# Kernel tuning notes

Measured on AMD Instinct MI355X. Metric: run time of the kernel, lower is better.

The kernel has to match this reference:

```python
import jax, jax.numpy as jnp
import numpy as np

B, N, DIN, DINNER, DOUT, W = 4, 8192, 512, 512, 512, 128


def setup_inputs() -> dict:
    key = jax.random.key(0)
    k1, k2, k3 = jax.random.split(key, 3)
    x = jax.random.normal(k1, (B, N, DIN), jnp.float32)
    # torch Linear weights: (out_features, in_features)
    w_qkv = jax.random.normal(k2, (3 * DINNER, DIN), jnp.float32) * (DIN ** -0.5)
    w_out = jax.random.normal(k3, (DOUT, DINNER), jnp.float32) * (DINNER ** -0.5)
    b_out = jnp.zeros((DOUT,), jnp.float32)
    return {"x": x, "w_qkv": w_qkv, "w_out": w_out, "b_out": b_out}


def reference(x, w_qkv, w_out, b_out):
    b, n, _ = x.shape
    w = W
    scale = DINNER ** -0.5
    pad = (-n) % w  # pad_to_multiple along seq dim (static)
    xp = jnp.pad(x, ((0, 0), (0, pad), (0, 0)))
    qkv = jnp.einsum('bnd,ed->bne', xp, w_qkv)  # to_qkv, no bias
    q, k, v = jnp.split(qkv, 3, axis=-1)
    win = lambda t: t.reshape(b, -1, w, DINNER)  # b (w n) d -> b w n d
    q, k, v = win(q), win(k), win(v)
    # prepend one zero bucket to k, then overlap prev/current windows.
    kp = jnp.pad(k, ((0, 0), (1, 0), (0, 0), (0, 0)))
    k2 = jnp.concatenate((kp[:, :-1], kp[:, 1:]), axis=2)  # (b, nb, 2w, d)
    # NOTE: source bug replicated — v is also built from k, not v.
    v2 = jnp.concatenate((kp[:, :-1], kp[:, 1:]), axis=2)
    sim = jnp.einsum('bwid,bwjd->bwij', q, k2) * scale  # (b, nb, w, 2w)
    i, j = w, 2 * w
    mask = jnp.triu(jnp.ones((i, j), bool), j - i + 1)
    sim = jnp.where(mask, -jnp.finfo(sim.dtype).max, sim)
    attn = jax.nn.softmax(sim, axis=-1)
    out = jnp.einsum('bwij,bwjd->bwid', attn, v2)
    out = out.reshape(b, -1, DINNER)[:, :n]
    return jnp.einsum('bnd,od->bno', out, w_out) + b_out
```

## Files before the change

kernel.cpp:

```cpp
#include <hip/hip_runtime.h>
#include <cstdint>
#include <cstddef>

typedef float f32x4 __attribute__((ext_vector_type(4)));
typedef short s16x8 __attribute__((ext_vector_type(8)));
typedef short s16x4 __attribute__((ext_vector_type(4)));

#define MFMA_BF16(a, b, c) __builtin_amdgcn_mfma_f32_16x16x32_bf16((a), (b), (c), 0, 0, 0)

#define GLD16(g, l)                                                            \
  __builtin_amdgcn_global_load_lds(                                            \
      (const __attribute__((address_space(1))) void*)(g),                      \
      (__attribute__((address_space(3))) void*)(l), 16, 0, 0)

__device__ __forceinline__ unsigned short f2bf(float f) {
  unsigned int u = __float_as_uint(f);
  u += 0x7FFFu + ((u >> 16) & 1u);
  return (unsigned short)(u >> 16);
}

__device__ __forceinline__ s16x8 cvt8(const float* __restrict__ src) {
  const float4 f0 = *(const float4*)src;
  const float4 f1 = *(const float4*)(src + 4);
  s16x8 h;
  h[0] = (short)f2bf(f0.x); h[1] = (short)f2bf(f0.y);
  h[2] = (short)f2bf(f0.z); h[3] = (short)f2bf(f0.w);
  h[4] = (short)f2bf(f1.x); h[5] = (short)f2bf(f1.y);
  h[6] = (short)f2bf(f1.z); h[7] = (short)f2bf(f1.w);
  return h;
}

#define XN 16777216
#define WQN 524288
__global__ __launch_bounds__(256)
void cvt_bf16(const float* __restrict__ x, const float* __restrict__ wqkv,
              const float* __restrict__ wout, unsigned short* __restrict__ xb,
              unsigned short* __restrict__ wb, unsigned short* __restrict__ wob) {
  const size_t i = (size_t)(blockIdx.x * 256 + threadIdx.x) * 8;
  const float* src;
  unsigned short* dst;
  if (i < XN) { src = x + i; dst = xb + i; }
  else if (i < XN + WQN) { src = wqkv + (i - XN); dst = wb + (i - XN); }
  else { src = wout + (i - XN - WQN); dst = wob + (i - XN - WQN); }
  *(s16x8*)dst = cvt8(src);
}

__global__ __launch_bounds__(256)
void gemm_qk(const unsigned short* __restrict__ xb, const unsigned short* __restrict__ wb,
             unsigned short* __restrict__ Q, unsigned short* __restrict__ K) {
  __shared__ unsigned short As[128 * 64];
  __shared__ unsigned short Bs[128 * 64];
  const int t = threadIdx.x, lane = t & 63, wid = t >> 6;
  const int wm = wid >> 1, wn = wid & 1;
  const int nl = lane & 15, quad = lane >> 4;
  const int sub = lane >> 3, lblk = (lane & 7) ^ sub;
  const int l = blockIdx.x;
  const int xcd = l & 7, g = l >> 3;
  const int mt = (g >> 3) * 8 + xcd, nt = g & 7;
  const int m0 = mt * 128, n0 = nt * 128;

  const f32x4 zero = {0.f, 0.f, 0.f, 0.f};
  f32x4 acc[4][4];
#pragma unroll
  for (int i = 0; i < 4; ++i)
#pragma unroll
    for (int j = 0; j < 4; ++j) acc[i][j] = zero;

  const unsigned short* gX = xb + (size_t)(m0 + wid * 32 + sub) * 512 + lblk * 8;
  const unsigned short* gW = wb + (size_t)(n0 + wid * 32 + sub) * 512 + lblk * 8;

  for (int kc = 0; kc < 512; kc += 64) {
#pragma unroll
    for (int ii = 0; ii < 4; ++ii) {
      GLD16(gW + kc + (size_t)(ii * 8) * 512, &As[(wid * 32 + ii * 8) * 64]);
      GLD16(gX + kc + (size_t)(ii * 8) * 512, &Bs[(wid * 32 + ii * 8) * 64]);
    }
    __syncthreads();
#pragma unroll
    for (int ks = 0; ks < 2; ++ks) {
      s16x8 af[4], bf[4];
#pragma unroll
      for (int i = 0; i < 4; ++i)
        af[i] = *(const s16x8*)&As[(wm * 64 + i * 16 + nl) * 64 +
                                   (((ks * 4 + quad) ^ (nl & 7)) * 8)];
#pragma unroll
      for (int j = 0; j < 4; ++j)
        bf[j] = *(const s16x8*)&Bs[(wn * 64 + j * 16 + nl) * 64 +
                                   (((ks * 4 + quad) ^ (nl & 7)) * 8)];
#pragma unroll
      for (int i = 0; i < 4; ++i)
#pragma unroll
        for (int j = 0; j < 4; ++j) acc[i][j] = MFMA_BF16(af[i], bf[j], acc[i][j]);
    }
    __syncthreads();
  }
#pragma unroll
  for (int i = 0; i < 4; ++i) {
    const int n = n0 + wm * 64 + i * 16 + quad * 4;
    unsigned short* base = (n < 512 ? Q : K);
    const int nn = n & 511;
#pragma unroll
    for (int j = 0; j < 4; ++j) {
      const int m = m0 + wn * 64 + j * 16 + nl;
      s16x4 h;
#pragma unroll
      for (int r = 0; r < 4; ++r) h[r] = (short)f2bf(acc[i][j][r]);
      *(s16x4*)&base[(size_t)m * 512 + nn] = h;
    }
  }
}

__global__ __launch_bounds__(256)
void gemm_kwt(const unsigned short* __restrict__ K, const unsigned short* __restrict__ wob,
              unsigned short* __restrict__ KWT) {
  __shared__ unsigned short As[128 * 64];
  __shared__ unsigned short Bs[128 * 64];
  const int t = threadIdx.x, lane = t & 63, wid = t >> 6;
  const int wm = wid >> 1, wn = wid & 1;
  const int nl = lane & 15, quad = lane >> 4;
  const int sub = lane >> 3, lblk = (lane & 7) ^ sub;
  const int l = blockIdx.x;
  const int xcd = l & 7, g = l >> 3;
  const int mt = (g >> 2) * 8 + xcd, nt = g & 3;
  const int m0 = mt * 128, n0 = nt * 128;

  const f32x4 zero = {0.f, 0.f, 0.f, 0.f};
  f32x4 acc[4][4];
#pragma unroll
  for (int i = 0; i < 4; ++i)
#pragma unroll
    for (int j = 0; j < 4; ++j) acc[i][j] = zero;

  const unsigned short* gA = K + (size_t)(m0 + wid * 32 + sub) * 512 + lblk * 8;
  const unsigned short* gB = wob + (size_t)(n0 + wid * 32 + sub) * 512 + lblk * 8;

  for (int kc = 0; kc < 512; kc += 64) {
#pragma unroll
    for (int ii = 0; ii < 4; ++ii) {
      GLD16(gA + kc + (size_t)(ii * 8) * 512, &As[(wid * 32 + ii * 8) * 64]);
      GLD16(gB + kc + (size_t)(ii * 8) * 512, &Bs[(wid * 32 + ii * 8) * 64]);
    }
    __syncthreads();
#pragma unroll
    for (int ks = 0; ks < 2; ++ks) {
      s16x8 af[4], bf[4];
#pragma unroll
      for (int i = 0; i < 4; ++i)
        af[i] = *(const s16x8*)&As[(wm * 64 + i * 16 + nl) * 64 +
                                   (((ks * 4 + quad) ^ (nl & 7)) * 8)];
#pragma unroll
      for (int j = 0; j < 4; ++j)
        bf[j] = *(const s16x8*)&Bs[(wn * 64 + j * 16 + nl) * 64 +
                                   (((ks * 4 + quad) ^ (nl & 7)) * 8)];
#pragma unroll
      for (int i = 0; i < 4; ++i)
#pragma unroll
        for (int j = 0; j < 4; ++j) acc[i][j] = MFMA_BF16(af[i], bf[j], acc[i][j]);
    }
    __syncthreads();
  }
#pragma unroll
  for (int i = 0; i < 4; ++i) {
    const int ms = m0 + wm * 64 + i * 16 + quad * 4;
    const int b = ms >> 13, ns = ms & 8191;
#pragma unroll
    for (int j = 0; j < 4; ++j) {
      const int o = n0 + wn * 64 + j * 16 + nl;
      s16x4 h;
#pragma unroll
      for (int r = 0; r < 4; ++r) h[r] = (short)f2bf(acc[i][j][r]);
      *(s16x4*)&KWT[(size_t)(b * 512 + o) * 8192 + ns] = h;
    }
  }
}

__global__ __launch_bounds__(256)
void attn64(const unsigned short* __restrict__ Q, const unsigned short* __restrict__ K,
            const unsigned short* __restrict__ KWT, const float* __restrict__ bias,
            float* __restrict__ out) {
  __shared__ __align__(16) char smem[73728];
  unsigned short* const Qb  = (unsigned short*)smem;
  unsigned short* const Kbo = (unsigned short*)(smem + 8192);
  unsigned short* const Kbe = (unsigned short*)(smem + 40960);
  unsigned short* const Ps  = (unsigned short*)smem;
  float* const redm = (float*)(smem + 32768);
  float* const reds = (float*)(smem + 33792);
  unsigned short* const B20 = (unsigned short*)(smem + 40960);
  unsigned short* const B21 = (unsigned short*)(smem + 57344);

  const int t = threadIdx.x, lane = t & 63, wid = t >> 6;
  const int wn = wid;
  const int nl = lane & 15, quad = lane >> 4;
  const int sub = lane >> 3, lblk = (lane & 7) ^ sub;
  const int bx = blockIdx.x;
  const int xcd = bx & 7, half = (bx >> 3) & 1, g = bx >> 4;
  const int wb = g * 8 + xcd, b = wb >> 6, w = wb & 63;

  const unsigned short* Qg = Q + (size_t)(b * 8192 + w * 128 + half * 64) * 512;
  const unsigned short* Kg = K + (size_t)(b * 8192) * 512;
  const unsigned short* KWTb = KWT + (size_t)(b * 512) * 8192;
  const int seqbase = w * 128 - 128;

#define STAGE_Q(kcc)                                                           \
  do {                                                                         \
    _Pragma("unroll") for (int ii = 0; ii < 2; ++ii)                           \
        GLD16(Qg + (size_t)(wid * 16 + ii * 8 + sub) * 512 + (kcc) + lblk * 8, \
              Qb + (wid * 16 + ii * 8) * 64);                                  \
  } while (0)

#define STAGE_K(kcc, kb)                                                       \
  do {                                                                         \
    _Pragma("unroll") for (int ii = 0; ii < 8; ++ii) {                         \
      int sq_ = seqbase + wid * 64 + ii * 8 + sub;                             \
      if (sq_ < 0) sq_ = 0;                                                    \
      GLD16(Kg + (size_t)sq_ * 512 + (kcc) + lblk * 8,                         \
            (kb) + (wid * 64 + ii * 8) * 64);                                  \
    }                                                                          \
  } while (0)

#define STAGE_B2(tt, bb)                                                       \
  do {                                                                         \
    const int och_ = (tt) >> 2, kch_ = (tt) & 3;                               \
    int sq_ = seqbase + kch_ * 64 + lblk * 8;                                  \
    if (sq_ < 0) sq_ = 0;                                                      \
    _Pragma("unroll") for (int ii = 0; ii < 4; ++ii)                           \
        GLD16(KWTb + (size_t)(och_ * 128 + wid * 32 + ii * 8 + sub) * 8192 + sq_, \
              (bb) + (wid * 32 + ii * 8) * 64);                                \
  } while (0)

  float bo[4][2];
#pragma unroll
  for (int och = 0; och < 4; ++och)
#pragma unroll
    for (int j = 0; j < 2; ++j) bo[och][j] = bias[och * 128 + wn * 32 + j * 16 + nl];

  const f32x4 zero = {0.f, 0.f, 0.f, 0.f};
  f32x4 acc[4][4];
#pragma unroll
  for (int i = 0; i < 4; ++i)
#pragma unroll
    for (int j = 0; j < 4; ++j) acc[i][j] = zero;

  STAGE_K(0, Kbe);
  STAGE_Q(0);
#pragma unroll
  for (int s = 0; s < 8; ++s) {
    unsigned short* const kb = (s & 1) ? Kbo : Kbe;
    if (s < 7) {
      STAGE_K((s + 1) * 64, (s & 1) ? Kbe : Kbo);
      asm volatile("s_waitcnt vmcnt(8)" ::: "memory");
    } else {
      STAGE_B2(0, B20);
      asm volatile("s_waitcnt vmcnt(4)" ::: "memory");
    }
    __builtin_amdgcn_s_barrier();
    asm volatile("" ::: "memory");
#pragma unroll
    for (int ks = 0; ks < 2; ++ks) {
      s16x8 af[4], bf[4];
#pragma unroll
      for (int i = 0; i < 4; ++i)
        af[i] = *(const s16x8*)&Qb[(i * 16 + nl) * 64 +
                                   (((ks * 4 + quad) ^ (nl & 7)) * 8)];
#pragma unroll
      for (int j = 0; j < 4; ++j)
        bf[j] = *(const s16x8*)&kb[(wn * 64 + j * 16 + nl) * 64 +
                                   (((ks * 4 + quad) ^ (nl & 7)) * 8)];
      __builtin_amdgcn_s_setprio(1);
#pragma unroll
      for (int i = 0; i < 4; ++i)
#pragma unroll
        for (int j = 0; j < 4; ++j) acc[i][j] = MFMA_BF16(af[i], bf[j], acc[i][j]);
      __builtin_amdgcn_s_setprio(0);
    }
    asm volatile("" ::: "memory");
    __builtin_amdgcn_s_barrier();
    if (s < 7) STAGE_Q((s + 1) * 64);
  }
  STAGE_B2(1, B21);

  const float scale = 0.04419417382415922f;
  float rmax[4][4];
#pragma unroll
  for (int i = 0; i < 4; ++i) {
#pragma unroll
    for (int r = 0; r < 4; ++r) {
      const int qrow = half * 64 + i * 16 + quad * 4 + r;
      float mx = -3.4e38f;
#pragma unroll
      for (int j = 0; j < 4; ++j) {
        const int col = wn * 64 + j * 16 + nl;
        float v = acc[i][j][r] * scale;
        if (col >= 128 && col - 128 > qrow) v = -3.0e38f;
        if (w == 0 && col < 128) v = 0.0f;
        acc[i][j][r] = v;
        mx = fmaxf(mx, v);
      }
      rmax[i][r] = mx;
    }
  }
#pragma unroll
  for (int off = 1; off < 16; off <<= 1)
#pragma unroll
    for (int i = 0; i < 4; ++i)
#pragma unroll
      for (int r = 0; r < 4; ++r)
        rmax[i][r] = fmaxf(rmax[i][r], __shfl_xor(rmax[i][r], off, 64));
  if (nl == 0) {
#pragma unroll
    for (int i = 0; i < 4; ++i)
#pragma unroll
      for (int r = 0; r < 4; ++r)
        redm[(i * 16 + quad * 4 + r) * 4 + wn] = rmax[i][r];
  }
  asm volatile("s_waitcnt lgkmcnt(0)" ::: "memory");
  __builtin_amdgcn_s_barrier();
  asm volatile("" ::: "memory");
  float rsum[4][4];
#pragma unroll
  for (int i = 0; i < 4; ++i) {
#pragma unroll
    for (int r = 0; r < 4; ++r) {
      const f32x4 mv = *(const f32x4*)&redm[(i * 16 + quad * 4 + r) * 4];
      const float m = fmaxf(fmaxf(mv[0], mv[1]), fmaxf(mv[2], mv[3]));
      float s = 0.f;
#pragma unroll
      for (int j = 0; j < 4; ++j) {
        const float p = __expf(acc[i][j][r] - m);
        acc[i][j][r] = p;
        s += p;
      }
      rsum[i][r] = s;
    }
  }
#pragma unroll
  for (int off = 1; off < 16; off <<= 1)
#pragma unroll
    for (int i = 0; i < 4; ++i)
#pragma unroll
      for (int r = 0; r < 4; ++r) rsum[i][r] += __shfl_xor(rsum[i][r], off, 64);
  if (nl == 0) {
#pragma unroll
    for (int i = 0; i < 4; ++i)
#pragma unroll
      for (int r = 0; r < 4; ++r)
        reds[(i * 16 + quad * 4 + r) * 4 + wn] = rsum[i][r];
  }
  asm volatile("s_waitcnt lgkmcnt(0)" ::: "memory");
  __builtin_amdgcn_s_barrier();
  asm volatile("" ::: "memory");
  float invv[4][4];
#pragma unroll
  for (int i = 0; i < 4; ++i)
#pragma unroll
    for (int r = 0; r < 4; ++r) {
      const f32x4 sv = *(const f32x4*)&reds[(i * 16 + quad * 4 + r) * 4];
      invv[i][r] = 1.0f / (sv[0] + sv[1] + sv[2] + sv[3]);
    }
  asm volatile("s_waitcnt lgkmcnt(0)" ::: "memory");
  __builtin_amdgcn_s_barrier();
  asm volatile("" ::: "memory");
#pragma unroll
  for (int i = 0; i < 4; ++i) {
#pragma unroll
    for (int r = 0; r < 4; ++r) {
      const int row = i * 16 + quad * 4 + r;
#pragma unroll
      for (int j = 0; j < 4; ++j) {
        const int col = wn * 64 + j * 16 + nl;
        float pv = acc[i][j][r] * invv[i][r];
        if (w == 0 && col < 128) pv = 0.0f;
        const int cb = col >> 3;
        Ps[row * 256 + (((cb ^ (row & 7)) << 3) | (col & 7))] = f2bf(pv);
      }
    }
  }
  asm volatile("s_waitcnt lgkmcnt(0)" ::: "memory");
  __builtin_amdgcn_s_barrier();
  asm volatile("" ::: "memory");

  f32x4 acc2[4][2];
#pragma unroll
  for (int t2 = 0; t2 < 16; ++t2) {
    const int och = t2 >> 2, kch = t2 & 3;
    unsigned short* const bb = (t2 & 1) ? B21 : B20;
    if (kch == 0) {
#pragma unroll
      for (int i = 0; i < 4; ++i)
#pragma unroll
        for (int j = 0; j < 2; ++j) acc2[i][j] = zero;
    }
    if (t2 < 15) asm volatile("s_waitcnt vmcnt(4)" ::: "memory");
    else         asm volatile("s_waitcnt vmcnt(0)" ::: "memory");
    __builtin_amdgcn_s_barrier();
    asm volatile("" ::: "memory");
#pragma unroll
    for (int ks = 0; ks < 2; ++ks) {
      const int kb2 = kch * 8 + ks * 4 + quad;
      s16x8 af[4], bf[2];
#pragma unroll
      for (int i = 0; i < 4; ++i)
        af[i] = *(const s16x8*)&Ps[(i * 16 + nl) * 256 + ((kb2 ^ (nl & 7)) << 3)];
#pragma unroll
      for (int j = 0; j < 2; ++j)
        bf[j] = *(const s16x8*)&bb[(wn * 32 + j * 16 + nl) * 64 +
                                   (((ks * 4 + quad) ^ (nl & 7)) * 8)];
      __builtin_amdgcn_s_setprio(1);
#pragma unroll
      for (int i = 0; i < 4; ++i) {
        acc2[i][0] = MFMA_BF16(af[i], bf[0], acc2[i][0]);
        acc2[i][1] = MFMA_BF16(af[i], bf[1], acc2[i][1]);
      }
      __builtin_amdgcn_s_setprio(0);
    }
    asm volatile("" ::: "memory");
    __builtin_amdgcn_s_barrier();
    if (kch == 3) {
#pragma unroll
      for (int i = 0; i < 4; ++i) {
        const int seq = w * 128 + half * 64 + i * 16 + quad * 4;
        float* dst = out + (size_t)(b * 8192 + seq) * 512;
#pragma unroll
        for (int j = 0; j < 2; ++j) {
          const int o = och * 128 + wn * 32 + j * 16 + nl;
#pragma unroll
          for (int r = 0; r < 4; ++r) dst[(size_t)r * 512 + o] = acc2[i][j][r] + bo[och][j];
        }
      }
    }
    if (t2 < 14) STAGE_B2(t2 + 2, bb);
  }
#undef STAGE_Q
#undef STAGE_K
#undef STAGE_B2
}

extern "C" void kernel_launch(void* const* d_in, const int* in_sizes, int n_in,
                              void* d_out, int out_size, void* d_ws, size_t ws_size,
                              hipStream_t stream) {
  const float* x = (const float*)d_in[0];
  const float* w_qkv = (const float*)d_in[1];
  const float* w_out = (const float*)d_in[2];
  const float* b_out = (const float*)d_in[3];
  float* out = (float*)d_out;

  char* ws = (char*)d_ws;
  unsigned short* Q = (unsigned short*)ws;
  unsigned short* K = (unsigned short*)(ws + (size_t)33554432);
  unsigned short* xb = (unsigned short*)(ws + (size_t)67108864);
  unsigned short* KWT = (unsigned short*)(ws + (size_t)67108864);
  unsigned short* wb = (unsigned short*)(ws + (size_t)100663296);
  unsigned short* wob = (unsigned short*)(ws + (size_t)100663296 + 1048576);

  cvt_bf16<<<dim3(8576), dim3(256), 0, stream>>>(x, w_qkv, w_out, xb, wb, wob);
  gemm_qk<<<dim3(2048), dim3(256), 0, stream>>>(xb, wb, Q, K);
  gemm_kwt<<<dim3(1024), dim3(256), 0, stream>>>(K, wob, KWT);
  attn64<<<dim3(512), dim3(256), 0, stream>>>(Q, K, KWT, b_out, out);
}
```

Baseline: 234.5 us.

## Fuse fp32-to-bf16 conversion of x into QK GEMM with register prefetch

The separate pass that converted x to bf16 is removed. The QK GEMM now loads fp32 x directly into registers, converts it, and writes it into LDS, prefetching the next K-chunk while the current one computes. The weight-only conversion stays as a small kernel. This saves a full write and re-read of a 32 MB bf16 copy of x, but each GEMM block now re-reads fp32 x once per N-tile (8 tiles), adds conversion ALU work and register pressure inside the GEMM, and uses manual waitcnt and barriers plus setprio around the MFMAs.

```diff
diff --git a/kernel.cpp b/kernel.cpp
--- a/kernel.cpp
+++ b/kernel.cpp
@@ -30,23 +30,29 @@
   return h;
 }
 
-#define XN 16777216
+__device__ __forceinline__ s16x8 cvt8r(float4 f0, float4 f1) {
+  s16x8 h;
+  h[0] = (short)f2bf(f0.x); h[1] = (short)f2bf(f0.y);
+  h[2] = (short)f2bf(f0.z); h[3] = (short)f2bf(f0.w);
+  h[4] = (short)f2bf(f1.x); h[5] = (short)f2bf(f1.y);
+  h[6] = (short)f2bf(f1.z); h[7] = (short)f2bf(f1.w);
+  return h;
+}
+
 #define WQN 524288
 __global__ __launch_bounds__(256)
-void cvt_bf16(const float* __restrict__ x, const float* __restrict__ wqkv,
-              const float* __restrict__ wout, unsigned short* __restrict__ xb,
-              unsigned short* __restrict__ wb, unsigned short* __restrict__ wob) {
+void cvt_w(const float* __restrict__ wqkv, const float* __restrict__ wout,
+           unsigned short* __restrict__ wb, unsigned short* __restrict__ wob) {
   const size_t i = (size_t)(blockIdx.x * 256 + threadIdx.x) * 8;
   const float* src;
   unsigned short* dst;
-  if (i < XN) { src = x + i; dst = xb + i; }
-  else if (i < XN + WQN) { src = wqkv + (i - XN); dst = wb + (i - XN); }
-  else { src = wout + (i - XN - WQN); dst = wob + (i - XN - WQN); }
+  if (i < WQN) { src = wqkv + i; dst = wb + i; }
+  else { src = wout + (i - WQN); dst = wob + (i - WQN); }
   *(s16x8*)dst = cvt8(src);
 }
 
 __global__ __launch_bounds__(256)
-void gemm_qk(const unsigned short* __restrict__ xb, const unsigned short* __restrict__ wb,
+void gemm_qk(const float* __restrict__ x, const unsigned short* __restrict__ wb,
              unsigned short* __restrict__ Q, unsigned short* __restrict__ K) {
   __shared__ unsigned short As[128 * 64];
   __shared__ unsigned short Bs[128 * 64];
@@ -66,16 +72,36 @@
 #pragma unroll
     for (int j = 0; j < 4; ++j) acc[i][j] = zero;
 
-  const unsigned short* gX = xb + (size_t)(m0 + wid * 32 + sub) * 512 + lblk * 8;
+  const float* gXf = x + (size_t)(m0 + wid * 32 + sub) * 512 + lblk * 8;
   const unsigned short* gW = wb + (size_t)(n0 + wid * 32 + sub) * 512 + lblk * 8;
 
+  float4 rx[4][2];
+#define LOADX(kcc)                                                             \
+  do {                                                                         \
+    _Pragma("unroll") for (int ii = 0; ii < 4; ++ii) {                         \
+      const float* p_ = gXf + (kcc) + ii * 4096;             \
+      rx[ii][0] = *(const float4*)p_;                                          \
+      rx[ii][1] = *(const float4*)(p_ + 4);                                    \
+    }                                                                          \
+  } while (0)
+
+  LOADX(0);
   for (int kc = 0; kc < 512; kc += 64) {
 #pragma unroll
-    for (int ii = 0; ii < 4; ++ii) {
+    for (int ii = 0; ii < 4; ++ii)
       GLD16(gW + kc + (size_t)(ii * 8) * 512, &As[(wid * 32 + ii * 8) * 64]);
-      GLD16(gX + kc + (size_t)(ii * 8) * 512, &Bs[(wid * 32 + ii * 8) * 64]);
-    }
-    __syncthreads();
+#pragma unroll
+    for (int ii = 0; ii < 4; ++ii)
+      *(s16x8*)&Bs[(wid * 32 + ii * 8 + sub) * 64 + (lane & 7) * 8] =
+          cvt8r(rx[ii][0], rx[ii][1]);
+    if (kc < 448) {
+      LOADX(kc + 64);
+      asm volatile("s_waitcnt vmcnt(8) lgkmcnt(0)" ::: "memory");
+    } else {
+      asm volatile("s_waitcnt vmcnt(0) lgkmcnt(0)" ::: "memory");
+    }
+    __builtin_amdgcn_s_barrier();
+    asm volatile("" ::: "memory");
 #pragma unroll
     for (int ks = 0; ks < 2; ++ks) {
       s16x8 af[4], bf[4];
@@ -87,13 +113,17 @@
       for (int j = 0; j < 4; ++j)
         bf[j] = *(const s16x8*)&Bs[(wn * 64 + j * 16 + nl) * 64 +
                                    (((ks * 4 + quad) ^ (nl & 7)) * 8)];
+      __builtin_amdgcn_s_setprio(1);
 #pragma unroll
       for (int i = 0; i < 4; ++i)
 #pragma unroll
         for (int j = 0; j < 4; ++j) acc[i][j] = MFMA_BF16(af[i], bf[j], acc[i][j]);
-    }
-    __syncthreads();
-  }
+      __builtin_amdgcn_s_setprio(0);
+    }
+    asm volatile("" ::: "memory");
+    __builtin_amdgcn_s_barrier();
+  }
+#undef LOADX
 #pragma unroll
   for (int i = 0; i < 4; ++i) {
     const int n = n0 + wm * 64 + i * 16 + quad * 4;
@@ -447,13 +477,12 @@
   char* ws = (char*)d_ws;
   unsigned short* Q = (unsigned short*)ws;
   unsigned short* K = (unsigned short*)(ws + (size_t)33554432);
-  unsigned short* xb = (unsigned short*)(ws + (size_t)67108864);
   unsigned short* KWT = (unsigned short*)(ws + (size_t)67108864);
   unsigned short* wb = (unsigned short*)(ws + (size_t)100663296);
   unsigned short* wob = (unsigned short*)(ws + (size_t)100663296 + 1048576);
 
-  cvt_bf16<<<dim3(8576), dim3(256), 0, stream>>>(x, w_qkv, w_out, xb, wb, wob);
-  gemm_qk<<<dim3(2048), dim3(256), 0, stream>>>(xb, wb, Q, K);
+  cvt_w<<<dim3(384), dim3(256), 0, stream>>>(w_qkv, w_out, wb, wob);
+  gemm_qk<<<dim3(2048), dim3(256), 0, stream>>>(x, wb, Q, K);
   gemm_kwt<<<dim3(1024), dim3(256), 0, stream>>>(K, wob, KWT);
   attn64<<<dim3(512), dim3(256), 0, stream>>>(Q, K, KWT, b_out, out);
 }
```

Measured after the change: 245.9 us. +4.8%, slower.
